# Kernel tuning notes

Hardware: AMD Instinct MI355X
Metric: run time of the kernel (lower is better)

## Reference

```python
import jax, jax.numpy as jnp
import numpy as np

HIDDEN = 2048
INTER = 768
N_EXPERTS = 16
TOP_K = 2
B, S = 4, 2048


def setup_inputs() -> dict:
    key = jax.random.key(0)
    ks = jax.random.split(key, 5)
    scale = 0.02
    return {
        "hidden_states": jax.random.normal(ks[0], (B, S, HIDDEN), dtype=jnp.float32),
        # nn.Linear weight layout: [out_features, in_features]
        "gate_w": jax.random.normal(ks[1], (N_EXPERTS, HIDDEN), dtype=jnp.float32) * scale,
        "w_gate": jax.random.normal(ks[2], (N_EXPERTS, INTER, HIDDEN), dtype=jnp.float32) * scale,
        "w_up": jax.random.normal(ks[3], (N_EXPERTS, INTER, HIDDEN), dtype=jnp.float32) * scale,
        "w_down": jax.random.normal(ks[4], (N_EXPERTS, HIDDEN, INTER), dtype=jnp.float32) * scale,
    }


def _moe_forward(hidden_states, gate_w, w_gate, w_up, w_down):
    b, s, h = hidden_states.shape
    x = hidden_states.reshape(-1, h)                      # [T, H]
    t = x.shape[0]
    logits = x @ gate_w.T                                 # [T, E]
    probs = jax.nn.softmax(logits, axis=-1)
    top_vals, top_idx = jax.lax.top_k(probs, TOP_K)       # [T, K]
    top_vals = top_vals / jnp.sum(top_vals, axis=-1, keepdims=True)
    # combine weights per token per expert (zero if not routed)
    comb = jnp.zeros((t, N_EXPERTS), dtype=x.dtype)
    comb = comb.at[jnp.arange(t)[:, None], top_idx].add(top_vals)  # [T, E]

    out = jnp.zeros_like(x)
    for e in range(N_EXPERTS):  # small fixed loop over experts
        g = x @ w_gate[e].T                               # [T, I]
        u = x @ w_up[e].T                                 # [T, I]
        y = (jax.nn.silu(g) * u) @ w_down[e].T            # [T, H]
        out = out + comb[:, e:e + 1] * y
    return out.reshape(b, s, h)


def reference(hidden_states, gate_w, w_gate, w_up, w_down):
    return _moe_forward(hidden_states, gate_w, w_gate, w_up, w_down)
```

## Files before the change

kernel.cpp:

```cpp
#include <hip/hip_runtime.h>
#include <hip/hip_bf16.h>

#define NTOK 8192
#define HID 2048
#define INTER 768
#define NEXP 16

typedef __bf16 bf16x8 __attribute__((ext_vector_type(8)));
typedef float f32x4 __attribute__((ext_vector_type(4)));

typedef const __attribute__((address_space(1))) void gvoid_t;
typedef __attribute__((address_space(3))) void lvoid_t;

static __device__ __forceinline__ void load_lds16(const void* g, void* l) {
  __builtin_amdgcn_global_load_lds((gvoid_t*)g, (lvoid_t*)l, 16, 0, 0);
}

static __device__ __forceinline__ unsigned short f2bf(float f) {
  unsigned int u = __float_as_uint(f);
  u += 0x7FFFu + ((u >> 16) & 1u);
  return (unsigned short)(u >> 16);
}

static __device__ __forceinline__ float bf2f(unsigned short b) {
  return __uint_as_float(((unsigned int)b) << 16);
}

__global__ __launch_bounds__(256) void cvt_kernel(const float* __restrict__ src,
                                                  unsigned short* __restrict__ dst, int n) {
  int i = (blockIdx.x * 256 + threadIdx.x) * 4;
  int stride = gridDim.x * 256 * 4;
  for (; i < n; i += stride) {
    float4 v = *reinterpret_cast<const float4*>(src + i);
    ushort4 o;
    o.x = f2bf(v.x); o.y = f2bf(v.y); o.z = f2bf(v.z); o.w = f2bf(v.w);
    *reinterpret_cast<ushort4*>(dst + i) = o;
  }
}

__global__ __launch_bounds__(256) void router_kernel(const float* __restrict__ x,
                                                     const float* __restrict__ gw,
                                                     int* __restrict__ te,
                                                     float* __restrict__ tw,
                                                     unsigned short* __restrict__ Xb) {
  const int lane = threadIdx.x & 63;
  const int wid = threadIdx.x >> 6;
  const int t0 = (blockIdx.x * 4 + wid) * 2;
  const float4* xa = reinterpret_cast<const float4*>(x + (size_t)t0 * HID);
  const float4* xb = xa + HID / 4;
  const float4* g4 = reinterpret_cast<const float4*>(gw);

  float4 va[8], vb[8];
#pragma unroll
  for (int j = 0; j < 8; ++j) {
    va[j] = xa[lane + 64 * j];
    vb[j] = xb[lane + 64 * j];
  }
  ushort4* oa = reinterpret_cast<ushort4*>(Xb + (size_t)t0 * HID);
  ushort4* ob = oa + HID / 4;
#pragma unroll
  for (int j = 0; j < 8; ++j) {
    ushort4 u;
    u.x = f2bf(va[j].x); u.y = f2bf(va[j].y); u.z = f2bf(va[j].z); u.w = f2bf(va[j].w);
    oa[lane + 64 * j] = u;
    u.x = f2bf(vb[j].x); u.y = f2bf(vb[j].y); u.z = f2bf(vb[j].z); u.w = f2bf(vb[j].w);
    ob[lane + 64 * j] = u;
  }

  float accA[NEXP], accB[NEXP];
#pragma unroll
  for (int e = 0; e < NEXP; ++e) { accA[e] = 0.f; accB[e] = 0.f; }
#pragma unroll
  for (int e = 0; e < NEXP; ++e) {
#pragma unroll
    for (int j = 0; j < 8; ++j) {
      float4 g = g4[e * (HID / 4) + lane + 64 * j];
      accA[e] += va[j].x * g.x + va[j].y * g.y + va[j].z * g.z + va[j].w * g.w;
      accB[e] += vb[j].x * g.x + vb[j].y * g.y + vb[j].z * g.z + vb[j].w * g.w;
    }
  }
#pragma unroll
  for (int e = 0; e < NEXP; ++e) {
#pragma unroll
    for (int m = 32; m >= 1; m >>= 1) {
      accA[e] += __shfl_xor(accA[e], m);
      accB[e] += __shfl_xor(accB[e], m);
    }
  }
  if (lane == 0) {
#pragma unroll
    for (int k = 0; k < 2; ++k) {
      const float* acc = k ? accB : accA;
      int t = t0 + k;
      float b0 = -1e30f; int i0 = 0;
#pragma unroll
      for (int e = 0; e < NEXP; ++e) { if (acc[e] > b0) { b0 = acc[e]; i0 = e; } }
      float b1 = -1e30f; int i1 = 0;
#pragma unroll
      for (int e = 0; e < NEXP; ++e) { if (e != i0 && acc[e] > b1) { b1 = acc[e]; i1 = e; } }
      float w0 = 1.f / (1.f + __expf(b1 - b0));
      te[2 * t] = i0; te[2 * t + 1] = i1;
      tw[2 * t] = w0; tw[2 * t + 1] = 1.f - w0;
    }
  }
}

__global__ __launch_bounds__(256) void build_kernel(
    const int* __restrict__ te, const float* __restrict__ tw,
    int* __restrict__ counts, int* __restrict__ offsets,
    int* __restrict__ tok_flat, float* __restrict__ w_flat,
    int* __restrict__ tile_map, int* __restrict__ n_tiles) {
  __shared__ int lds_cnt[NEXP][257];
  __shared__ int lds_off[NEXP];
  const int tid = threadIdx.x;
  const int lane = tid & 63;
  const int wv = tid >> 6;

  int cnt[NEXP];
#pragma unroll
  for (int ex = 0; ex < NEXP; ++ex) cnt[ex] = 0;
  for (int i = 0; i < 64; ++i) {
    int e = te[tid * 64 + i];
#pragma unroll
    for (int ex = 0; ex < NEXP; ++ex) cnt[ex] += (e == ex) ? 1 : 0;
  }
#pragma unroll
  for (int ex = 0; ex < NEXP; ++ex) lds_cnt[ex][tid] = cnt[ex];
  __syncthreads();

  for (int ex = wv * 4; ex < wv * 4 + 4; ++ex) {
    int carry = 0;
    for (int c = 0; c < 4; ++c) {
      int v = lds_cnt[ex][c * 64 + lane];
      int s = v;
#pragma unroll
      for (int d = 1; d < 64; d <<= 1) {
        int o = __shfl_up(s, d);
        if (lane >= d) s += o;
      }
      lds_cnt[ex][c * 64 + lane] = carry + s - v;
      carry += __shfl(s, 63);
    }
    if (lane == 0) lds_cnt[ex][256] = carry;
  }
  __syncthreads();

  if (tid == 0) {
    int run = 0, nt = 0;
    for (int e = 0; e < NEXP; ++e) {
      int tot = lds_cnt[e][256];
      counts[e] = tot;
      offsets[e] = run;
      lds_off[e] = run;
      for (int m0 = 0; m0 < tot; m0 += 128) tile_map[nt++] = (e << 16) | m0;
      run += tot;
    }
    *n_tiles = nt;
  }
  __syncthreads();

  int base[NEXP];
#pragma unroll
  for (int ex = 0; ex < NEXP; ++ex) base[ex] = lds_off[ex] + lds_cnt[ex][tid];
  for (int i = 0; i < 64; ++i) {
    int idx = tid * 64 + i;
    int e = te[idx];
    float w = tw[idx];
    int pos = 0;
#pragma unroll
    for (int ex = 0; ex < NEXP; ++ex) {
      if (e == ex) { pos = base[ex]; base[ex] = pos + 1; }
    }
    tok_flat[pos] = idx >> 1;
    w_flat[pos] = w;
  }
}

#define EP_G 0
#define EP_U 1
#define EP_D 2

template <int MODE, int NXB, int KD>
__global__ __launch_bounds__(256, 3) void gemm_kernel(
    const unsigned short* __restrict__ A,
    const unsigned short* __restrict__ Bw,
    const int* __restrict__ counts, const int* __restrict__ offsets,
    const int* __restrict__ tok_flat, const float* __restrict__ w_flat,
    const int* __restrict__ tile_map, const int* __restrict__ n_tiles,
    unsigned short* __restrict__ Hf, float* __restrict__ out) {
  const int bid = blockIdx.x;
  const int cpx = gridDim.x >> 3;
  const int wg = (bid & 7) * cpx + (bid >> 3);
  const int y = wg / NXB;
  if (y >= *n_tiles) return;
  const int xb = wg - y * NXB;
  const int tm = tile_map[y];
  const int e = tm >> 16, m0 = tm & 0xFFFF;
  const int cnt = counts[e];
  const int off = offsets[e];
  const int n0 = xb * 128;

  __shared__ __align__(16) unsigned short As0[128 * 32], As1[128 * 32];
  __shared__ __align__(16) unsigned short Bs0[128 * 32], Bs1[128 * 32];

  const int tid = threadIdx.x;
  const int lane = tid & 63;
  const int wid = tid >> 6;
  const int rl = tid >> 2;
  const int srcc = ((tid & 3) ^ ((tid >> 3) & 3)) * 8;
  const int d0 = tid * 8;
  const int d1 = d0 + 64 * 32;

  const int r0 = m0 + rl, r1 = r0 + 64;
  const int s0 = (r0 < cnt) ? off + r0 : off;
  const int s1 = (r1 < cnt) ? off + r1 : off;
  const unsigned short* aptr0;
  const unsigned short* aptr1;
  if (MODE == EP_D) {
    aptr0 = A + (size_t)s0 * KD + srcc;
    aptr1 = A + (size_t)s1 * KD + srcc;
  } else {
    aptr0 = A + (size_t)tok_flat[s0] * KD + srcc;
    aptr1 = A + (size_t)tok_flat[s1] * KD + srcc;
  }
  const unsigned short* bptr0 = Bw + ((size_t)e * (NXB * 128) + n0 + rl) * KD + srcc;
  const unsigned short* bptr1 = bptr0 + (size_t)64 * KD;

  f32x4 zero = {0.f, 0.f, 0.f, 0.f};
  f32x4 acc[4][4];
#pragma unroll
  for (int i = 0; i < 4; ++i)
#pragma unroll
    for (int j = 0; j < 4; ++j) acc[i][j] = zero;

  const int wm = (wid >> 1) * 64;
  const int wn = (wid & 1) * 64;
  const int fr = lane & 15;
  const int cs = (((lane >> 4) ^ ((lane >> 1) & 3)) * 8);

#define STAGE(AS, BS, kt)                 \
  {                                       \
    load_lds16(aptr0 + (kt), (AS) + d0);  \
    load_lds16(aptr1 + (kt), (AS) + d1);  \
    load_lds16(bptr0 + (kt), (BS) + d0);  \
    load_lds16(bptr1 + (kt), (BS) + d1);  \
  }

#define COMPUTE(AS, BS)                                                                \
  {                                                                                    \
    bf16x8 af[4], bf_[4];                                                              \
    _Pragma("unroll") for (int i = 0; i < 4; ++i) {                                    \
      af[i] = *reinterpret_cast<const bf16x8*>((AS) + (wm + i * 16 + fr) * 32 + cs);   \
      bf_[i] = *reinterpret_cast<const bf16x8*>((BS) + (wn + i * 16 + fr) * 32 + cs);  \
    }                                                                                  \
    _Pragma("unroll") for (int i = 0; i < 4; ++i)                                      \
      _Pragma("unroll") for (int j = 0; j < 4; ++j)                                    \
        acc[i][j] = __builtin_amdgcn_mfma_f32_16x16x32_bf16(af[i], bf_[j], acc[i][j], 0, 0, 0); \
  }

  STAGE(As0, Bs0, 0);
  __syncthreads();
#pragma unroll 1
  for (int kt = 0; kt < KD; kt += 64) {
    STAGE(As1, Bs1, kt + 32);
    COMPUTE(As0, Bs0);
    __syncthreads();
    if (kt + 64 < KD) STAGE(As0, Bs0, kt + 64);
    COMPUTE(As1, Bs1);
    __syncthreads();
  }
#undef STAGE
#undef COMPUTE

  const int lr = (lane >> 4) * 4;
  const int lc = lane & 15;
#pragma unroll
  for (int i = 0; i < 4; ++i) {
#pragma unroll
    for (int r = 0; r < 4; ++r) {
      int m = wm + i * 16 + lr + r;
      if (m0 + m < cnt) {
        int slot = off + m0 + m;
        if (MODE == EP_G) {
          size_t base = (size_t)slot * INTER + (size_t)(n0 + wn + lc);
#pragma unroll
          for (int j = 0; j < 4; ++j) Hf[base + j * 16] = f2bf(acc[i][j][r]);
        } else if (MODE == EP_U) {
          size_t base = (size_t)slot * INTER + (size_t)(n0 + wn + lc);
#pragma unroll
          for (int j = 0; j < 4; ++j) {
            float g = bf2f(Hf[base + j * 16]);
            float u = acc[i][j][r];
            float h = g / (1.f + __expf(-g)) * u;
            Hf[base + j * 16] = f2bf(h);
          }
        } else {
          int t = tok_flat[slot];
          float w = w_flat[slot];
          float* op = out + (size_t)t * HID + (size_t)(n0 + wn + lc);
#pragma unroll
          for (int j = 0; j < 4; ++j) atomicAdd(op + j * 16, w * acc[i][j][r]);
        }
      }
    }
  }
}

extern "C" void kernel_launch(void* const* d_in, const int* in_sizes, int n_in,
                              void* d_out, int out_size, void* d_ws, size_t ws_size,
                              hipStream_t stream) {
  const float* x  = (const float*)d_in[0];
  const float* gw = (const float*)d_in[1];
  const float* wg = (const float*)d_in[2];
  const float* wu = (const float*)d_in[3];
  const float* wd = (const float*)d_in[4];
  float* out = (float*)d_out;
  char* ws = (char*)d_ws;

  int*   counts   = (int*)(ws + 0);
  int*   offsets  = (int*)(ws + 128);
  int*   n_tiles  = (int*)(ws + 192);
  int*   tile_map = (int*)(ws + 256);
  int*   te       = (int*)(ws + 1024);
  float* tw       = (float*)(ws + 66560);
  int*   tok_flat = (int*)(ws + 132096);
  float* w_flat   = (float*)(ws + 197632);
  unsigned short* Xb  = (unsigned short*)(ws + 263168);
  unsigned short* Wgb = (unsigned short*)(ws + 33817600);
  unsigned short* Wub = (unsigned short*)(ws + 84149248);
  unsigned short* Wdb = (unsigned short*)(ws + 134480896);
  unsigned short* Hf  = (unsigned short*)(ws + 184812544);

  hipMemsetAsync(d_out, 0, (size_t)NTOK * HID * sizeof(float), stream);

  cvt_kernel<<<2048, 256, 0, stream>>>(wg, Wgb, NEXP * INTER * HID);
  cvt_kernel<<<2048, 256, 0, stream>>>(wu, Wub, NEXP * INTER * HID);
  cvt_kernel<<<2048, 256, 0, stream>>>(wd, Wdb, NEXP * HID * INTER);

  router_kernel<<<NTOK / 8, 256, 0, stream>>>(x, gw, te, tw, Xb);
  build_kernel<<<1, 256, 0, stream>>>(te, tw, counts, offsets, tok_flat, w_flat,
                                      tile_map, n_tiles);

  gemm_kernel<EP_G, 6, HID><<<144 * 6, 256, 0, stream>>>(
      Xb, Wgb, counts, offsets, tok_flat, w_flat, tile_map, n_tiles, Hf, out);
  gemm_kernel<EP_U, 6, HID><<<144 * 6, 256, 0, stream>>>(
      Xb, Wub, counts, offsets, tok_flat, w_flat, tile_map, n_tiles, Hf, out);
  gemm_kernel<EP_D, 16, INTER><<<144 * 16, 256, 0, stream>>>(
      Hf, Wdb, counts, offsets, tok_flat, w_flat, tile_map, n_tiles, Hf, out);
}
```

Baseline: 516.3 us.

## Replace atomic scatter in down GEMM with bf16 slot buffer and combine kernel

The down-projection GEMM now writes its routing-weighted results as bf16 into a per-slot buffer that reuses the gate weight workspace, instead of doing fp32 atomicAdds into the output. A new combine kernel uses a token-to-slot map built by build_kernel to sum each token's two expert rows and write the output. This removes the output memset and the atomic traffic. The GEMM main loop is also restructured to stage both K halves before one barrier, which drops the overlap of loads with compute. It adds a bf16 rounding step on the per-expert outputs and an extra kernel launch with its own memory pass.

```diff
diff --git a/kernel.cpp b/kernel.cpp
--- a/kernel.cpp
+++ b/kernel.cpp
@@ -109,6 +109,7 @@
     const int* __restrict__ te, const float* __restrict__ tw,
     int* __restrict__ counts, int* __restrict__ offsets,
     int* __restrict__ tok_flat, float* __restrict__ w_flat,
+    int* __restrict__ tok_slot,
     int* __restrict__ tile_map, int* __restrict__ n_tiles) {
   __shared__ int lds_cnt[NEXP][257];
   __shared__ int lds_off[NEXP];
@@ -173,12 +174,13 @@
     }
     tok_flat[pos] = idx >> 1;
     w_flat[pos] = w;
+    tok_slot[idx] = pos;
   }
 }
 
 #define EP_G 0
 #define EP_U 1
-#define EP_D 2
+#define EP_Y 2
 
 template <int MODE, int NXB, int KD>
 __global__ __launch_bounds__(256, 3) void gemm_kernel(
@@ -216,7 +218,7 @@
   const int s1 = (r1 < cnt) ? off + r1 : off;
   const unsigned short* aptr0;
   const unsigned short* aptr1;
-  if (MODE == EP_D) {
+  if (MODE == EP_Y) {
     aptr0 = A + (size_t)s0 * KD + srcc;
     aptr1 = A + (size_t)s1 * KD + srcc;
   } else {
@@ -258,14 +260,12 @@
         acc[i][j] = __builtin_amdgcn_mfma_f32_16x16x32_bf16(af[i], bf_[j], acc[i][j], 0, 0, 0); \
   }
 
-  STAGE(As0, Bs0, 0);
-  __syncthreads();
 #pragma unroll 1
   for (int kt = 0; kt < KD; kt += 64) {
+    STAGE(As0, Bs0, kt);
     STAGE(As1, Bs1, kt + 32);
+    __syncthreads();
     COMPUTE(As0, Bs0);
-    __syncthreads();
-    if (kt + 64 < KD) STAGE(As0, Bs0, kt + 64);
     COMPUTE(As1, Bs1);
     __syncthreads();
   }
@@ -295,15 +295,39 @@
             Hf[base + j * 16] = f2bf(h);
           }
         } else {
-          int t = tok_flat[slot];
           float w = w_flat[slot];
-          float* op = out + (size_t)t * HID + (size_t)(n0 + wn + lc);
-#pragma unroll
-          for (int j = 0; j < 4; ++j) atomicAdd(op + j * 16, w * acc[i][j][r]);
+          size_t base = (size_t)slot * HID + (size_t)(n0 + wn + lc);
+#pragma unroll
+          for (int j = 0; j < 4; ++j) Hf[base + j * 16] = f2bf(w * acc[i][j][r]);
         }
       }
     }
   }
+}
+
+__global__ __launch_bounds__(256) void combine_kernel(const unsigned short* __restrict__ Yf,
+                                                      const int* __restrict__ tok_slot,
+                                                      float* __restrict__ out) {
+  const int t = blockIdx.x;
+  const int c = threadIdx.x * 8;
+  const int s0 = tok_slot[2 * t];
+  const int s1 = tok_slot[2 * t + 1];
+  const ushort4* p0 = reinterpret_cast<const ushort4*>(Yf + (size_t)s0 * HID + c);
+  const ushort4* p1 = reinterpret_cast<const ushort4*>(Yf + (size_t)s1 * HID + c);
+  ushort4 a0 = p0[0], a1 = p0[1];
+  ushort4 b0 = p1[0], b1 = p1[1];
+  float4 o0, o1;
+  o0.x = bf2f(a0.x) + bf2f(b0.x);
+  o0.y = bf2f(a0.y) + bf2f(b0.y);
+  o0.z = bf2f(a0.z) + bf2f(b0.z);
+  o0.w = bf2f(a0.w) + bf2f(b0.w);
+  o1.x = bf2f(a1.x) + bf2f(b1.x);
+  o1.y = bf2f(a1.y) + bf2f(b1.y);
+  o1.z = bf2f(a1.z) + bf2f(b1.z);
+  o1.w = bf2f(a1.w) + bf2f(b1.w);
+  float4* op = reinterpret_cast<float4*>(out + (size_t)t * HID + c);
+  op[0] = o0;
+  op[1] = o1;
 }
 
 extern "C" void kernel_launch(void* const* d_in, const int* in_sizes, int n_in,
@@ -330,8 +354,8 @@
   unsigned short* Wub = (unsigned short*)(ws + 84149248);
   unsigned short* Wdb = (unsigned short*)(ws + 134480896);
   unsigned short* Hf  = (unsigned short*)(ws + 184812544);
-
-  hipMemsetAsync(d_out, 0, (size_t)NTOK * HID * sizeof(float), stream);
+  int*   tok_slot = (int*)(ws + 209978368);
+  unsigned short* Yf  = Wgb;
 
   cvt_kernel<<<2048, 256, 0, stream>>>(wg, Wgb, NEXP * INTER * HID);
   cvt_kernel<<<2048, 256, 0, stream>>>(wu, Wub, NEXP * INTER * HID);
@@ -339,12 +363,13 @@
 
   router_kernel<<<NTOK / 8, 256, 0, stream>>>(x, gw, te, tw, Xb);
   build_kernel<<<1, 256, 0, stream>>>(te, tw, counts, offsets, tok_flat, w_flat,
-                                      tile_map, n_tiles);
+                                      tok_slot, tile_map, n_tiles);
 
   gemm_kernel<EP_G, 6, HID><<<144 * 6, 256, 0, stream>>>(
       Xb, Wgb, counts, offsets, tok_flat, w_flat, tile_map, n_tiles, Hf, out);
   gemm_kernel<EP_U, 6, HID><<<144 * 6, 256, 0, stream>>>(
       Xb, Wub, counts, offsets, tok_flat, w_flat, tile_map, n_tiles, Hf, out);
-  gemm_kernel<EP_D, 16, INTER><<<144 * 16, 256, 0, stream>>>(
-      Hf, Wdb, counts, offsets, tok_flat, w_flat, tile_map, n_tiles, Hf, out);
-}
+  gemm_kernel<EP_Y, 16, INTER><<<144 * 16, 256, 0, stream>>>(
+      Hf, Wdb, counts, offsets, tok_flat, w_flat, tile_map, n_tiles, Yf, out);
+  combine_kernel<<<NTOK, 256, 0, stream>>>(Yf, tok_slot, out);
+}
```

Measured after the change: 484.8 us. 6.1% less time.
